# Kernel optimization log

Hardware: AMD Instinct MI355X
Metric: run time of the kernel (lower is better)

Reference implementation:

```python
import jax, jax.numpy as jnp
import numpy as np
from jax import lax

K_SIZE = 5  # dilated_kernel_size


def dcls_kernel(w, p, k=K_SIZE):
    """Build dense (Cout,Cin,k,k) kernel from DCLS v1 bilinear interpolation.
    w: (Cout,Cin,Kc) weights; p: (2,Cout,Cin,Kc) learnable positions."""
    lim = k // 2
    pos = jnp.clip(p, -lim, lim) + lim          # in [0, k-1]
    i = jnp.floor(pos).astype(jnp.int32)
    r = pos - i                                  # bilinear fractions
    Co, Ci, Kc = w.shape
    co = jnp.arange(Co)[:, None, None]
    ci = jnp.arange(Ci)[None, :, None]
    i1, i2 = i[0], i[1]
    r1, r2 = r[0], r[1]
    # scatter into (k+1)x(k+1) grid so i+1 never goes out of bounds, then trim
    K = jnp.zeros((Co, Ci, k + 1, k + 1), w.dtype)
    K = K.at[co, ci, i1,     i2    ].add(w * (1 - r1) * (1 - r2))
    K = K.at[co, ci, i1 + 1, i2    ].add(w * r1 * (1 - r2))
    K = K.at[co, ci, i1,     i2 + 1].add(w * (1 - r1) * r2)
    K = K.at[co, ci, i1 + 1, i2 + 1].add(w * r1 * r2)
    return K[:, :, :k, :k]


def conv2d(x, K, pad):
    return lax.conv_general_dilated(
        x, K, window_strides=(1, 1), padding=[(pad, pad), (pad, pad)],
        dimension_numbers=('NCHW', 'OIHW', 'NCHW'))


def maxpool2(x):
    return lax.reduce_window(x, -jnp.inf, lax.max, (1, 1, 2, 2), (1, 1, 2, 2), 'VALID')


def setup_inputs() -> dict:
    key = jax.random.key(0)
    ks = jax.random.split(key, 12)
    lim = K_SIZE // 2
    B = 4096
    x = jax.random.normal(ks[0], (B, 1, 28, 28), jnp.float32)
    w1 = jax.random.normal(ks[1], (32, 1, 16), jnp.float32) * 0.2
    p1 = jax.random.uniform(ks[2], (2, 32, 1, 16), jnp.float32, -lim, lim)
    b1 = jnp.zeros((32,), jnp.float32)
    w2 = jax.random.normal(ks[3], (64, 32, 32), jnp.float32) * 0.05
    p2 = jax.random.uniform(ks[4], (2, 64, 32, 32), jnp.float32, -lim, lim)
    b2 = jnp.zeros((64,), jnp.float32)
    fc1_w = jax.random.normal(ks[5], (128, 64 * 7 * 7), jnp.float32) * 0.02
    fc1_b = jnp.zeros((128,), jnp.float32)
    fc2_w = jax.random.normal(ks[6], (10, 128), jnp.float32) * 0.08
    fc2_b = jnp.zeros((10,), jnp.float32)
    return dict(x=x, w1=w1, p1=p1, b1=b1, w2=w2, p2=p2, b2=b2,
                fc1_w=fc1_w, fc1_b=fc1_b, fc2_w=fc2_w, fc2_b=fc2_b)


def reference(x, w1, p1, b1, w2, p2, b2, fc1_w, fc1_b, fc2_w, fc2_b):
    h = conv2d(x, dcls_kernel(w1, p1), pad=2) + b1[None, :, None, None]
    h = maxpool2(jax.nn.relu(h))                       # (B,32,14,14)
    h = conv2d(h, dcls_kernel(w2, p2), pad=2) + b2[None, :, None, None]
    h = maxpool2(jax.nn.relu(h))                       # (B,64,7,7)
    h = h.reshape(-1, 64 * 7 * 7)
    h = jax.nn.relu(h @ fc1_w.T + fc1_b)
    return h @ fc2_w.T + fc2_b                         # (B,10)
```

## Files before the change

### kernel.cpp

```cpp
#include <hip/hip_runtime.h>
#include <hip/hip_bf16.h>

typedef __attribute__((ext_vector_type(8))) short short8;
typedef __attribute__((ext_vector_type(4))) short short4v;
typedef __attribute__((ext_vector_type(4))) float float4v;
typedef __attribute__((ext_vector_type(16))) float float16v;

static __device__ __forceinline__ unsigned short f2bf(float f) {
    unsigned u = __float_as_uint(f);
    unsigned r = (u + 0x7FFF + ((u >> 16) & 1)) >> 16;
    return (unsigned short)r;
}

__global__ __launch_bounds__(256) void prep_all(
    const float* __restrict__ w1, const float* __restrict__ p1,
    const float* __restrict__ w2, const float* __restrict__ p2,
    const float* __restrict__ fc1w,
    unsigned short* __restrict__ K1b,
    unsigned short* __restrict__ Kt,
    unsigned short* __restrict__ w1b) {
    const int blk = blockIdx.x;
    const int t = threadIdx.x;

    if (blk < 8) {
        int cell = blk * 256 + t;
        int co = cell >> 6;
        int k = cell & 63;
        int wr = k >> 3;
        int kx = k & 7;
        float acc = 0.f;
        if (wr < 5 && kx < 5) {
#pragma unroll 8
            for (int kc = 0; kc < 16; ++kc) {
                float wv = w1[co * 16 + kc];
                float pa = p1[co * 16 + kc];
                float pb = p1[512 + co * 16 + kc];
                float pos1 = fminf(fmaxf(pa, -2.f), 2.f) + 2.f;
                float pos2 = fminf(fmaxf(pb, -2.f), 2.f) + 2.f;
                int i1 = (int)floorf(pos1);
                int i2 = (int)floorf(pos2);
                float r1 = pos1 - (float)i1;
                float r2 = pos2 - (float)i2;
                float c = 0.f;
                if (i1 == wr && i2 == kx) c += (1.f - r1) * (1.f - r2);
                if (i1 + 1 == wr && i2 == kx) c += r1 * (1.f - r2);
                if (i1 == wr && i2 + 1 == kx) c += (1.f - r1) * r2;
                if (i1 + 1 == wr && i2 + 1 == kx) c += r1 * r2;
                acc += wv * c;
            }
        }
        K1b[cell] = f2bf(acc);
    } else if (blk < 208) {
        int cell = (blk - 8) * 256 + t;
        int kk = cell >> 11;
        int co = (cell >> 5) & 63;
        int ci = cell & 31;
        int ky = kk / 5;
        int kx = kk - 5 * ky;
        const int base = (co * 32 + ci) * 32;
        float acc = 0.f;
#pragma unroll 8
        for (int kc = 0; kc < 32; ++kc) {
            float wv = w2[base + kc];
            float pa = p2[base + kc];
            float pb = p2[65536 + base + kc];
            float pos1 = fminf(fmaxf(pa, -2.f), 2.f) + 2.f;
            float pos2 = fminf(fmaxf(pb, -2.f), 2.f) + 2.f;
            int i1 = (int)floorf(pos1);
            int i2 = (int)floorf(pos2);
            float r1 = pos1 - (float)i1;
            float r2 = pos2 - (float)i2;
            float c = 0.f;
            if (i1 == ky && i2 == kx) c += (1.f - r1) * (1.f - r2);
            if (i1 + 1 == ky && i2 == kx) c += r1 * (1.f - r2);
            if (i1 == ky && i2 + 1 == kx) c += (1.f - r1) * r2;
            if (i1 + 1 == ky && i2 + 1 == kx) c += r1 * r2;
            acc += wv * c;
        }
        Kt[cell] = f2bf(acc);
    } else {
        int i8 = ((blk - 208) * 256 + t) * 8;
        float4 v0 = *(const float4*)(fc1w + i8);
        float4 v1 = *(const float4*)(fc1w + i8 + 4);
        short8 o = {(short)f2bf(v0.x), (short)f2bf(v0.y), (short)f2bf(v0.z),
                    (short)f2bf(v0.w), (short)f2bf(v1.x), (short)f2bf(v1.y),
                    (short)f2bf(v1.z), (short)f2bf(v1.w)};
        *(short8*)(w1b + i8) = o;
    }
}

__global__ __launch_bounds__(256, 4) void fused_conv_mfma(
    const float* __restrict__ x,
    const unsigned short* __restrict__ K1b,
    const unsigned short* __restrict__ Kt,
    const float* __restrict__ b1,
    const float* __restrict__ b2,
    unsigned short* __restrict__ h2) {
    __shared__ __align__(16) unsigned short h1p[18 * 20 * 40];
    __shared__ __align__(16) unsigned short smu[5888];

    unsigned short* sm4 = smu;
    unsigned short* sm_xb = smu + 5104;
    unsigned short* KtS = smu;

    const int b = blockIdx.x;
    const int tid = threadIdx.x;
    const int lane = tid & 63;
    const int wv = tid >> 6;
    const int n16 = lane & 15;
    const int cig = lane >> 4;

    const int yi = 2 * (n16 >> 3) + ((n16 >> 1) & 1);
    const int xi = 2 * ((n16 >> 2) & 1) + (n16 & 1);
    const int pYo = cig >> 1, pXo = cig & 1;

    const int mq = lane & 31;
    const int Qx = mq >> 2;
    const int dy2 = (mq >> 1) & 1;
    const int dx2 = mq & 1;
    const int hh = lane >> 5;

    const int g = wv * 64 + lane;
    const int stg_dst = (g >> 2) * 40 + (g & 3) * 8;
    const unsigned short* stg_src = Kt + g * 8;

    for (int t = tid; t < 1800; t += 256) ((uint4*)h1p)[t] = uint4{0, 0, 0, 0};
    {
        const float* xb = x + (size_t)b * 784;
        for (int t = tid; t < 784; t += 256) sm_xb[t] = f2bf(xb[t]);
    }
    __syncthreads();

    if (tid < 116) {
        int s = tid / 29;
        int r = tid - s * 29;
        unsigned short* dst = sm4 + (s * 29 + r) * 44;
        bool rok = r < 28;
#pragma unroll
        for (int g2 = 0; g2 < 11; ++g2) {
            short4v v;
#pragma unroll
            for (int e = 0; e < 4; ++e) {
                int c = g2 * 4 + e + s - 4;
                v[e] = (short)((rok && (unsigned)c < 28u) ? sm_xb[r * 28 + c]
                                                          : (unsigned short)0);
            }
            *(short4v*)(dst + g2 * 4) = v;
        }
    }

    short8 bw[2][2];
    float bias1[2], bias2n[2];
#pragma unroll
    for (int cot = 0; cot < 2; ++cot) {
#pragma unroll
        for (int h = 0; h < 2; ++h)
            bw[cot][h] = *(const short8*)(K1b + (cot * 16 + n16) * 64 + h * 32 + cig * 8);
        bias1[cot] = b1[cot * 16 + n16];
    }
#pragma unroll
    for (int nt = 0; nt < 2; ++nt) bias2n[nt] = b2[nt * 32 + mq];

    const int s1 = (xi + 2) & 3;
    const int pb1 = (xi + 2) & ~3;
    const unsigned short* a1base = sm4 + s1 * (29 * 44) + pb1;

    __syncthreads();

    for (int i = 0; i < 13; ++i) {
        int t = wv + 4 * i;
        if (t < 49) {
            int tY = t / 7, tX = t - 7 * tY;
            const unsigned short* ab = a1base + 4 * tX;
            int r0 = 4 * tY + yi - 2 + cig;
            int r1 = r0 + 4;
            int rr0 = ((unsigned)r0 < 28u) ? r0 : 28;
            int rr1 = ((unsigned)r1 < 28u) ? r1 : 28;
            short4v lo0 = *(const short4v*)(ab + rr0 * 44);
            short4v hi0 = *(const short4v*)(ab + rr0 * 44 + 4);
            short4v lo1 = *(const short4v*)(ab + rr1 * 44);
            short4v hi1 = *(const short4v*)(ab + rr1 * 44 + 4);
            short8 af0 = {lo0[0], lo0[1], lo0[2], lo0[3], hi0[0], hi0[1], hi0[2], hi0[3]};
            short8 af1 = {lo1[0], lo1[1], lo1[2], lo1[3], hi1[0], hi1[1], hi1[2], hi1[3]};
            int pY = 2 * tY + pYo, pX = 2 * tX + pXo;
#pragma unroll
            for (int cot = 0; cot < 2; ++cot) {
                float4v acc = {0.f, 0.f, 0.f, 0.f};
                acc = __builtin_amdgcn_mfma_f32_16x16x32_bf16(af0, bw[cot][0], acc, 0, 0, 0);
                acc = __builtin_amdgcn_mfma_f32_16x16x32_bf16(af1, bw[cot][1], acc, 0, 0, 0);
                float v = fmaxf(fmaxf(acc[0], acc[1]), fmaxf(acc[2], acc[3]));
                v = fmaxf(v + bias1[cot], 0.f);
                h1p[((pY + 2) * 20 + (pX + 2)) * 40 + cot * 16 + n16] = f2bf(v);
            }
        }
    }

    int x2 = 2 * Qx + dx2;
    if (x2 > 13) x2 = 13;
    int aoff[2][2];
    int pYv[2];
#pragma unroll
    for (int mt = 0; mt < 2; ++mt) {
        int pY = 2 * wv + mt;
        int y2 = 2 * pY + dy2;
        if (y2 > 13) y2 = 13;
        pYv[mt] = pY;
#pragma unroll
        for (int kh2 = 0; kh2 < 2; ++kh2)
            aoff[mt][kh2] = (y2 * 20 + x2) * 40 + kh2 * 16 + hh * 8;
    }

    float16v acc2[2][2];
#pragma unroll
    for (int mt = 0; mt < 2; ++mt)
#pragma unroll
        for (int nt = 0; nt < 2; ++nt)
#pragma unroll
            for (int e = 0; e < 16; ++e) acc2[mt][nt][e] = 0.f;

    const int wbase = mq * 40 + hh * 8;

    short8 stg0 = *(const short8*)(stg_src);
    __syncthreads();
    *(short8*)(KtS + stg_dst) = stg0;
    __syncthreads();

#pragma unroll
    for (int kk = 0; kk < 25; ++kk) {
        const int buf = kk & 1;
        short8 stg;
        if (kk < 24) stg = *(const short8*)(stg_src + (kk + 1) * 2048);

        const int ky = kk / 5;
        const int kx = kk - 5 * ky;
        const int soff = (ky * 20 + kx) * 40;
        short8 wff[2][2], aff[2][2];
#pragma unroll
        for (int nt = 0; nt < 2; ++nt)
#pragma unroll
            for (int q = 0; q < 2; ++q)
                wff[nt][q] = *(const short8*)(KtS + buf * 2560 + nt * 1280 +
                                              wbase + q * 16);
#pragma unroll
        for (int mt = 0; mt < 2; ++mt)
#pragma unroll
            for (int q = 0; q < 2; ++q)
                aff[mt][q] = *(const short8*)(h1p + aoff[mt][q] + soff);

        __builtin_amdgcn_sched_barrier(0);
#pragma unroll
        for (int mt = 0; mt < 2; ++mt)
#pragma unroll
            for (int nt = 0; nt < 2; ++nt) {
                acc2[mt][nt] = __builtin_amdgcn_mfma_f32_32x32x16_bf16(
                    aff[mt][0], wff[nt][0], acc2[mt][nt], 0, 0, 0);
                acc2[mt][nt] = __builtin_amdgcn_mfma_f32_32x32x16_bf16(
                    aff[mt][1], wff[nt][1], acc2[mt][nt], 0, 0, 0);
            }
        __builtin_amdgcn_sched_barrier(0);

        if (kk < 24) *(short8*)(KtS + (buf ^ 1) * 2560 + stg_dst) = stg;
        __syncthreads();
    }

    unsigned short* outb = h2 + (size_t)b * 3136;
#pragma unroll
    for (int mt = 0; mt < 2; ++mt) {
        if (pYv[mt] < 7) {
#pragma unroll
            for (int nt = 0; nt < 2; ++nt) {
#pragma unroll
                for (int g2 = 0; g2 < 4; ++g2) {
                    int pX = 2 * g2 + hh;
                    float v = fmaxf(fmaxf(acc2[mt][nt][4 * g2], acc2[mt][nt][4 * g2 + 1]),
                                    fmaxf(acc2[mt][nt][4 * g2 + 2], acc2[mt][nt][4 * g2 + 3]));
                    v = fmaxf(v + bias2n[nt], 0.f);
                    if (pX < 7)
                        outb[(nt * 32 + mq) * 49 + pYv[mt] * 7 + pX] = f2bf(v);
                }
            }
        }
    }
}

__global__ __launch_bounds__(256) void fc1_mfma(
    const unsigned short* __restrict__ A,
    const unsigned short* __restrict__ Wb,
    float* __restrict__ part, size_t PB) {
    __shared__ __align__(16) unsigned short As[64 * 72];
    const int blk = blockIdx.x;
    const int kh = blk % 7;
    const int m0 = (blk / 7) * 64;
    const int tid = threadIdx.x;
    const int wv = tid >> 6;
    const int lane = tid & 63;
    const int n16 = lane & 15;
    const int cig = lane >> 4;

    float4v acc[4][2];
#pragma unroll
    for (int mt = 0; mt < 4; ++mt)
#pragma unroll
        for (int j = 0; j < 2; ++j) acc[mt][j] = float4v{0.f, 0.f, 0.f, 0.f};

    for (int it = 0; it < 7; ++it) {
        int k0 = kh * 448 + it * 64;
        __syncthreads();
#pragma unroll
        for (int i = 0; i < 2; ++i) {
            int p = tid + 256 * i;
            int r = p >> 3, ko = (p & 7) * 8;
            *(short8*)(As + r * 72 + ko) =
                *(const short8*)(A + (size_t)(m0 + r) * 3136 + k0 + ko);
        }
        __syncthreads();
#pragma unroll
        for (int h = 0; h < 2; ++h) {
            short8 af[4];
#pragma unroll
            for (int mt = 0; mt < 4; ++mt)
                af[mt] = *(const short8*)(As + (mt * 16 + n16) * 72 + h * 32 + cig * 8);
            short8 wf[2];
#pragma unroll
            for (int j = 0; j < 2; ++j)
                wf[j] = *(const short8*)(Wb + (size_t)((wv * 2 + j) * 16 + n16) * 3136 +
                                         k0 + h * 32 + cig * 8);
#pragma unroll
            for (int mt = 0; mt < 4; ++mt)
#pragma unroll
                for (int j = 0; j < 2; ++j)
                    acc[mt][j] = __builtin_amdgcn_mfma_f32_16x16x32_bf16(
                        af[mt], wf[j], acc[mt][j], 0, 0, 0);
        }
    }
    float* o = part + (size_t)kh * PB;
#pragma unroll
    for (int mt = 0; mt < 4; ++mt)
#pragma unroll
        for (int j = 0; j < 2; ++j)
#pragma unroll
            for (int r = 0; r < 4; ++r) {
                int row = m0 + mt * 16 + cig * 4 + r;
                o[(size_t)row * 128 + (wv * 2 + j) * 16 + n16] = acc[mt][j][r];
            }
}

__global__ __launch_bounds__(256) void fc2_kernel(
    const float* __restrict__ part, size_t PB,
    const float* __restrict__ fc1b,
    const float* __restrict__ W, const float* __restrict__ bias,
    float* __restrict__ out) {
    __shared__ float smW[10 * 132];
    __shared__ float smB1[128];
    __shared__ float smB[10];
    int t = threadIdx.x;
    for (int i = t; i < 1280; i += 256) {
        int n = i >> 7, k = i & 127;
        smW[n * 132 + k] = W[i];
    }
    if (t < 128) smB1[t] = fc1b[t];
    if (t < 10) smB[t] = bias[t];
    __syncthreads();
    const int r = t >> 3;
    const int q = t & 7;
    const size_t b = (size_t)blockIdx.x * 32 + r;
    const float* pb = part + b * 128 + q * 16;

    float rv[16];
#pragma unroll
    for (int c = 0; c < 4; ++c) {
        float4 s = *(const float4*)(pb + 4 * c);
#pragma unroll
        for (int j = 1; j < 7; ++j) {
            float4 pj = *(const float4*)(pb + (size_t)j * PB + 4 * c);
            s.x += pj.x; s.y += pj.y; s.z += pj.z; s.w += pj.w;
        }
        float4 bv = *(const float4*)(smB1 + q * 16 + 4 * c);
        rv[4 * c + 0] = fmaxf(s.x + bv.x, 0.f);
        rv[4 * c + 1] = fmaxf(s.y + bv.y, 0.f);
        rv[4 * c + 2] = fmaxf(s.z + bv.z, 0.f);
        rv[4 * c + 3] = fmaxf(s.w + bv.w, 0.f);
    }
    float acc[10];
#pragma unroll
    for (int n = 0; n < 10; ++n) {
        const float4* wr = (const float4*)(smW + n * 132 + q * 16);
        float a = 0.f;
#pragma unroll
        for (int c = 0; c < 4; ++c) {
            float4 w = wr[c];
            a += rv[4 * c] * w.x + rv[4 * c + 1] * w.y +
                 rv[4 * c + 2] * w.z + rv[4 * c + 3] * w.w;
        }
        acc[n] = a;
    }
#pragma unroll
    for (int n = 0; n < 10; ++n) {
        acc[n] += __shfl_xor(acc[n], 1);
        acc[n] += __shfl_xor(acc[n], 2);
        acc[n] += __shfl_xor(acc[n], 4);
    }
    if (q == 0) {
#pragma unroll
        for (int n = 0; n < 10; ++n) out[b * 10 + n] = acc[n] + smB[n];
    }
}

extern "C" void kernel_launch(void* const* d_in, const int* in_sizes, int n_in,
                              void* d_out, int out_size, void* d_ws, size_t ws_size,
                              hipStream_t stream) {
    const float* x    = (const float*)d_in[0];
    const float* w1   = (const float*)d_in[1];
    const float* p1   = (const float*)d_in[2];
    const float* b1   = (const float*)d_in[3];
    const float* w2   = (const float*)d_in[4];
    const float* p2   = (const float*)d_in[5];
    const float* b2   = (const float*)d_in[6];
    const float* fc1w = (const float*)d_in[7];
    const float* fc1b = (const float*)d_in[8];
    const float* fc2w = (const float*)d_in[9];
    const float* fc2b = (const float*)d_in[10];
    float* out = (float*)d_out;

    const int B = in_sizes[0] / 784;

    float* ws = (float*)d_ws;
    unsigned short* Kt  = (unsigned short*)ws;
    unsigned short* K1b = (unsigned short*)(ws + 25600);
    unsigned short* w1b = (unsigned short*)(ws + 26624);
    unsigned short* h2b = (unsigned short*)(ws + 227328);
    float* fc1p = ws + 227328 + (size_t)B * 1568;

    prep_all<<<404, 256, 0, stream>>>(w1, p1, w2, p2, fc1w, K1b, Kt, w1b);
    fused_conv_mfma<<<B, 256, 0, stream>>>(x, K1b, Kt, b1, b2, h2b);
    fc1_mfma<<<(B / 64) * 7, 256, 0, stream>>>(h2b, w1b, fc1p, (size_t)B * 128);
    fc2_kernel<<<B / 32, 256, 0, stream>>>(fc1p, (size_t)B * 128,
                                           fc1b, fc2w, fc2b, out);
}
```

Before: 209.2 us.

## Triple-buffer conv2 weight staging and prefetch fragments into registers one step ahead

Conv2 weight slices in shared memory now rotate through three buffers instead of two, and global staging runs two taps ahead. Register fragments for the next tap are loaded from LDS while the MFMAs for the current tap run, with s_setprio raising wave priority around the MFMA block. The last iteration skips its barrier. In exchange the kernel uses more LDS and more registers, and the occupancy hint drops from 4 to 3 blocks per CU.

```diff
diff --git a/kernel.cpp b/kernel.cpp
--- a/kernel.cpp
+++ b/kernel.cpp
@@ -89,7 +89,7 @@
     }
 }
 
-__global__ __launch_bounds__(256, 4) void fused_conv_mfma(
+__global__ __launch_bounds__(256, 3) void fused_conv_mfma(
     const float* __restrict__ x,
     const unsigned short* __restrict__ K1b,
     const unsigned short* __restrict__ Kt,
@@ -97,7 +97,7 @@
     const float* __restrict__ b2,
     unsigned short* __restrict__ h2) {
     __shared__ __align__(16) unsigned short h1p[18 * 20 * 40];
-    __shared__ __align__(16) unsigned short smu[5888];
+    __shared__ __align__(16) unsigned short smu[7680];
 
     unsigned short* sm4 = smu;
     unsigned short* sm_xb = smu + 5104;
@@ -221,46 +221,67 @@
     const int wbase = mq * 40 + hh * 8;
 
     short8 stg0 = *(const short8*)(stg_src);
+    short8 stg1 = *(const short8*)(stg_src + 2048);
     __syncthreads();
     *(short8*)(KtS + stg_dst) = stg0;
+    *(short8*)(KtS + 2560 + stg_dst) = stg1;
     __syncthreads();
 
+    short8 wfp[2][2][2];
+    short8 afp[2][2][2];
+#pragma unroll
+    for (int nt = 0; nt < 2; ++nt)
+#pragma unroll
+        for (int q = 0; q < 2; ++q)
+            wfp[0][nt][q] = *(const short8*)(KtS + nt * 1280 + wbase + q * 16);
+#pragma unroll
+    for (int mt = 0; mt < 2; ++mt)
+#pragma unroll
+        for (int q = 0; q < 2; ++q)
+            afp[0][mt][q] = *(const short8*)(h1p + aoff[mt][q]);
+
 #pragma unroll
     for (int kk = 0; kk < 25; ++kk) {
-        const int buf = kk & 1;
+        const int cs = kk & 1;
+        const int ns = cs ^ 1;
         short8 stg;
-        if (kk < 24) stg = *(const short8*)(stg_src + (kk + 1) * 2048);
-
-        const int ky = kk / 5;
-        const int kx = kk - 5 * ky;
-        const int soff = (ky * 20 + kx) * 40;
-        short8 wff[2][2], aff[2][2];
-#pragma unroll
-        for (int nt = 0; nt < 2; ++nt)
-#pragma unroll
-            for (int q = 0; q < 2; ++q)
-                wff[nt][q] = *(const short8*)(KtS + buf * 2560 + nt * 1280 +
-                                              wbase + q * 16);
-#pragma unroll
-        for (int mt = 0; mt < 2; ++mt)
-#pragma unroll
-            for (int q = 0; q < 2; ++q)
-                aff[mt][q] = *(const short8*)(h1p + aoff[mt][q] + soff);
+        if (kk < 23) stg = *(const short8*)(stg_src + (kk + 2) * 2048);
+
+        if (kk < 24) {
+            const int kn = kk + 1;
+            const int ky = kn / 5;
+            const int kx = kn - 5 * ky;
+            const int soff = (ky * 20 + kx) * 40;
+            const int nbuf = (kn % 3) * 2560;
+#pragma unroll
+            for (int nt = 0; nt < 2; ++nt)
+#pragma unroll
+                for (int q = 0; q < 2; ++q)
+                    wfp[ns][nt][q] = *(const short8*)(KtS + nbuf + nt * 1280 +
+                                                      wbase + q * 16);
+#pragma unroll
+            for (int mt = 0; mt < 2; ++mt)
+#pragma unroll
+                for (int q = 0; q < 2; ++q)
+                    afp[ns][mt][q] = *(const short8*)(h1p + aoff[mt][q] + soff);
+        }
 
         __builtin_amdgcn_sched_barrier(0);
+        __builtin_amdgcn_s_setprio(1);
 #pragma unroll
         for (int mt = 0; mt < 2; ++mt)
 #pragma unroll
             for (int nt = 0; nt < 2; ++nt) {
                 acc2[mt][nt] = __builtin_amdgcn_mfma_f32_32x32x16_bf16(
-                    aff[mt][0], wff[nt][0], acc2[mt][nt], 0, 0, 0);
+                    afp[cs][mt][0], wfp[cs][nt][0], acc2[mt][nt], 0, 0, 0);
                 acc2[mt][nt] = __builtin_amdgcn_mfma_f32_32x32x16_bf16(
-                    aff[mt][1], wff[nt][1], acc2[mt][nt], 0, 0, 0);
-            }
+                    afp[cs][mt][1], wfp[cs][nt][1], acc2[mt][nt], 0, 0, 0);
+            }
+        __builtin_amdgcn_s_setprio(0);
         __builtin_amdgcn_sched_barrier(0);
 
-        if (kk < 24) *(short8*)(KtS + (buf ^ 1) * 2560 + stg_dst) = stg;
-        __syncthreads();
+        if (kk < 23) *(short8*)(KtS + ((kk + 2) % 3) * 2560 + stg_dst) = stg;
+        if (kk < 24) __syncthreads();
     }
 
     unsigned short* outb = h2 + (size_t)b * 3136;
```

After: 209.7 us. About the same (+0.2%).

## Load conv2 weights directly into registers in MFMA fragment layout, drop LDS staging

Applied to the files above, without the earlier changes.

The prep kernel now writes the conv2 weight tensor pre-permuted into the per-lane MFMA B-fragment order, so each lane can read its fragments straight from global memory. The main loop drops the LDS double buffer and the per-iteration __syncthreads, and instead double-buffers the weight fragments in registers, prefetching the next tap. It also raises MFMA wave priority with s_setprio and lowers the occupancy hint to 3 blocks. In exchange it uses more registers and repeats global/L2 weight reads in every wave, and with the shared buffer no longer aliased the LDS footprint grows.

```diff
diff --git a/kernel.cpp b/kernel.cpp
--- a/kernel.cpp
+++ b/kernel.cpp
@@ -77,7 +77,9 @@
             if (i1 + 1 == ky && i2 + 1 == kx) c += r1 * r2;
             acc += wv * c;
         }
-        Kt[cell] = f2bf(acc);
+        int nt = co >> 5, mq = co & 31;
+        int kh2 = ci >> 4, hh = (ci >> 3) & 1, jj = ci & 7;
+        Kt[kk * 2048 + nt * 1024 + kh2 * 512 + hh * 256 + mq * 8 + jj] = f2bf(acc);
     } else {
         int i8 = ((blk - 208) * 256 + t) * 8;
         float4 v0 = *(const float4*)(fc1w + i8);
@@ -89,7 +91,7 @@
     }
 }
 
-__global__ __launch_bounds__(256, 4) void fused_conv_mfma(
+__global__ __launch_bounds__(256, 3) void fused_conv_mfma(
     const float* __restrict__ x,
     const unsigned short* __restrict__ K1b,
     const unsigned short* __restrict__ Kt,
@@ -97,11 +99,8 @@
     const float* __restrict__ b2,
     unsigned short* __restrict__ h2) {
     __shared__ __align__(16) unsigned short h1p[18 * 20 * 40];
-    __shared__ __align__(16) unsigned short smu[5888];
-
-    unsigned short* sm4 = smu;
-    unsigned short* sm_xb = smu + 5104;
-    unsigned short* KtS = smu;
+    __shared__ __align__(16) unsigned short sm4[4 * 29 * 44];
+    __shared__ __align__(16) unsigned short sm_xb[784];
 
     const int b = blockIdx.x;
     const int tid = threadIdx.x;
@@ -119,10 +118,6 @@
     const int dy2 = (mq >> 1) & 1;
     const int dx2 = mq & 1;
     const int hh = lane >> 5;
-
-    const int g = wv * 64 + lane;
-    const int stg_dst = (g >> 2) * 40 + (g & 3) * 8;
-    const unsigned short* stg_src = Kt + g * 8;
 
     for (int t = tid; t < 1800; t += 256) ((uint4*)h1p)[t] = uint4{0, 0, 0, 0};
     {
@@ -218,29 +213,33 @@
 #pragma unroll
             for (int e = 0; e < 16; ++e) acc2[mt][nt][e] = 0.f;
 
-    const int wbase = mq * 40 + hh * 8;
-
-    short8 stg0 = *(const short8*)(stg_src);
+    const unsigned short* KtL = Kt + lane * 8;
+
+    short8 wfp[2][2][2];
+#pragma unroll
+    for (int nt = 0; nt < 2; ++nt)
+#pragma unroll
+        for (int q = 0; q < 2; ++q)
+            wfp[0][nt][q] = *(const short8*)(KtL + nt * 1024 + q * 512);
+
     __syncthreads();
-    *(short8*)(KtS + stg_dst) = stg0;
-    __syncthreads();
 
 #pragma unroll
     for (int kk = 0; kk < 25; ++kk) {
-        const int buf = kk & 1;
-        short8 stg;
-        if (kk < 24) stg = *(const short8*)(stg_src + (kk + 1) * 2048);
-
+        const int cs = kk & 1;
+        const int ns = cs ^ 1;
+        if (kk < 24) {
+#pragma unroll
+            for (int nt = 0; nt < 2; ++nt)
+#pragma unroll
+                for (int q = 0; q < 2; ++q)
+                    wfp[ns][nt][q] = *(const short8*)(KtL + (kk + 1) * 2048 +
+                                                      nt * 1024 + q * 512);
+        }
         const int ky = kk / 5;
         const int kx = kk - 5 * ky;
         const int soff = (ky * 20 + kx) * 40;
-        short8 wff[2][2], aff[2][2];
-#pragma unroll
-        for (int nt = 0; nt < 2; ++nt)
-#pragma unroll
-            for (int q = 0; q < 2; ++q)
-                wff[nt][q] = *(const short8*)(KtS + buf * 2560 + nt * 1280 +
-                                              wbase + q * 16);
+        short8 aff[2][2];
 #pragma unroll
         for (int mt = 0; mt < 2; ++mt)
 #pragma unroll
@@ -248,19 +247,18 @@
                 aff[mt][q] = *(const short8*)(h1p + aoff[mt][q] + soff);
 
         __builtin_amdgcn_sched_barrier(0);
+        __builtin_amdgcn_s_setprio(1);
 #pragma unroll
         for (int mt = 0; mt < 2; ++mt)
 #pragma unroll
             for (int nt = 0; nt < 2; ++nt) {
                 acc2[mt][nt] = __builtin_amdgcn_mfma_f32_32x32x16_bf16(
-                    aff[mt][0], wff[nt][0], acc2[mt][nt], 0, 0, 0);
+                    aff[mt][0], wfp[cs][nt][0], acc2[mt][nt], 0, 0, 0);
                 acc2[mt][nt] = __builtin_amdgcn_mfma_f32_32x32x16_bf16(
-                    aff[mt][1], wff[nt][1], acc2[mt][nt], 0, 0, 0);
-            }
+                    aff[mt][1], wfp[cs][nt][1], acc2[mt][nt], 0, 0, 0);
+            }
+        __builtin_amdgcn_s_setprio(0);
         __builtin_amdgcn_sched_barrier(0);
-
-        if (kk < 24) *(short8*)(KtS + (buf ^ 1) * 2560 + stg_dst) = stg;
-        __syncthreads();
     }
 
     unsigned short* outb = h2 + (size_t)b * 3136;
```

New measurement: 208.1 us. About the same (-0.5%).
